# Kernel tuning notes

Hardware: AMD Instinct MI355X
Metric: run time of the kernel (lower is better)

Reference implementation:

```python
import jax, jax.numpy as jnp
import numpy as np

N_NODES = 100000
N_EDGES = 1600000
IN_CH = 64
HID = 64
OUT_CH = 16
T = 1.0


def _gat_layer(x, edge_index, W, b, t):
    # x: [N, d_in]; W: [d_out, d_in] (torch Linear weight layout); b: [d_out]
    N = x.shape[0]
    loop = jnp.arange(N, dtype=edge_index.dtype)
    src = jnp.concatenate([edge_index[0], loop])  # add self loops
    dst = jnp.concatenate([edge_index[1], loop])
    h = x @ W.T  # [N, d_out]
    x_i = h[dst]  # target node features per edge
    x_j = h[src]  # source node features per edge
    alpha = jnp.sum(x_i * x_j, axis=-1)  # [E']
    alpha = jnp.where(alpha > 0, jnp.asarray(t, h.dtype), jnp.asarray(-t, h.dtype))
    # segment softmax grouped by edge_index[0] (source), faithful to original
    m = jax.ops.segment_max(alpha, src, num_segments=N)
    e = jnp.exp(alpha - m[src])
    s = jax.ops.segment_sum(e, src, num_segments=N)
    w = e / s[src]
    msg = x_j * w[:, None]
    out = jax.ops.segment_sum(msg, dst, num_segments=N)  # scatter-add to target
    return out + b


def setup_inputs() -> dict:
    key = jax.random.key(0)
    k1, k2, k3, k4 = jax.random.split(key, 4)
    x = jax.random.normal(k1, (N_NODES, IN_CH), dtype=jnp.float32)
    edge_index = jax.random.randint(k2, (2, N_EDGES), 0, N_NODES, dtype=jnp.int64)
    # xavier-uniform-ish linear weights, torch layout [out, in]
    lim1 = float(np.sqrt(6.0 / (IN_CH + HID)))
    W1 = jax.random.uniform(k3, (HID, IN_CH), jnp.float32, -lim1, lim1)
    lim2 = float(np.sqrt(6.0 / (HID + OUT_CH)))
    W2 = jax.random.uniform(k4, (OUT_CH, HID), jnp.float32, -lim2, lim2)
    b1 = jnp.zeros((HID,), jnp.float32)
    b2 = jnp.zeros((OUT_CH,), jnp.float32)
    return {"x": x, "edge_index": edge_index, "W1": W1, "b1": b1, "W2": W2, "b2": b2}


def reference(x, edge_index, W1, b1, W2, b2):
    h = _gat_layer(x, edge_index, W1, b1, T)
    h = jax.nn.relu(h)
    h = _gat_layer(h, edge_index, W2, b2, T)
    return jax.nn.log_softmax(h, axis=1)
```

## Files before the change

kernel.cpp:

```cpp
#include <hip/hip_runtime.h>

#define EXPC 0.13533528323661270f
#define REP 8
#define CHUNK 16384

__global__ void zero_i32(int* __restrict__ p, int n) {
  int i = blockIdx.x * blockDim.x + threadIdx.x;
  if (i < n) p[i] = 0;
}

template <bool RELU_IN>
__global__ void __launch_bounds__(256, 1)
gemm64_k(const float* __restrict__ x, const float* __restrict__ W,
         float* __restrict__ h, int N) {
  __shared__ float xs[64][68];
  __shared__ float wt[64][68];
  const int t = threadIdx.x;
  const int r0 = blockIdx.x * 64;
  for (int i = t; i < 4096; i += 256) {
    int c = i >> 6, k = i & 63;
    wt[k][c] = W[i];
  }
  for (int s = t; s < 1024; s += 256) {
    int r = s >> 4, c4 = (s & 15) << 2;
    float4 v = make_float4(0.f, 0.f, 0.f, 0.f);
    if (r0 + r < N) {
      v = *(const float4*)(x + (size_t)(r0 + r) * 64 + c4);
      if (RELU_IN) {
        v.x = fmaxf(v.x, 0.f); v.y = fmaxf(v.y, 0.f);
        v.z = fmaxf(v.z, 0.f); v.w = fmaxf(v.w, 0.f);
      }
    }
    *(float4*)(&xs[r][c4]) = v;
  }
  __syncthreads();
  const int ty = t >> 4, tx = t & 15;
  float acc[4][4] = {};
  for (int kk = 0; kk < 64; kk += 4) {
    float4 a[4], w[4];
#pragma unroll
    for (int i = 0; i < 4; i++) a[i] = *(const float4*)(&xs[4 * ty + i][kk]);
#pragma unroll
    for (int m = 0; m < 4; m++) w[m] = *(const float4*)(&wt[kk + m][4 * tx]);
#pragma unroll
    for (int i = 0; i < 4; i++) {
      acc[i][0] = fmaf(a[i].x, w[0].x, fmaf(a[i].y, w[1].x,
                  fmaf(a[i].z, w[2].x, fmaf(a[i].w, w[3].x, acc[i][0]))));
      acc[i][1] = fmaf(a[i].x, w[0].y, fmaf(a[i].y, w[1].y,
                  fmaf(a[i].z, w[2].y, fmaf(a[i].w, w[3].y, acc[i][1]))));
      acc[i][2] = fmaf(a[i].x, w[0].z, fmaf(a[i].y, w[1].z,
                  fmaf(a[i].z, w[2].z, fmaf(a[i].w, w[3].z, acc[i][2]))));
      acc[i][3] = fmaf(a[i].x, w[0].w, fmaf(a[i].y, w[1].w,
                  fmaf(a[i].z, w[2].w, fmaf(a[i].w, w[3].w, acc[i][3]))));
    }
  }
#pragma unroll
  for (int i = 0; i < 4; i++) {
    int row = r0 + 4 * ty + i;
    if (row < N)
      *(float4*)(h + (size_t)row * 64 + 4 * tx) =
          make_float4(acc[i][0], acc[i][1], acc[i][2], acc[i][3]);
  }
}

template <bool RELU_IN>
__global__ void __launch_bounds__(256, 2)
gemm16_k(const float* __restrict__ x, const float* __restrict__ W,
         float* __restrict__ h, int N) {
  __shared__ float xs[64][68];
  __shared__ float wt[64][20];
  const int t = threadIdx.x;
  const int r0 = blockIdx.x * 64;
  for (int i = t; i < 1024; i += 256) {
    int c = i >> 6, k = i & 63;
    wt[k][c] = W[i];
  }
  for (int s = t; s < 1024; s += 256) {
    int r = s >> 4, c4 = (s & 15) << 2;
    float4 v = make_float4(0.f, 0.f, 0.f, 0.f);
    if (r0 + r < N) {
      v = *(const float4*)(x + (size_t)(r0 + r) * 64 + c4);
      if (RELU_IN) {
        v.x = fmaxf(v.x, 0.f); v.y = fmaxf(v.y, 0.f);
        v.z = fmaxf(v.z, 0.f); v.w = fmaxf(v.w, 0.f);
      }
    }
    *(float4*)(&xs[r][c4]) = v;
  }
  __syncthreads();
  const int r = t >> 2, j = (t & 3) << 2;
  float4 acc = make_float4(0.f, 0.f, 0.f, 0.f);
  for (int k = 0; k < 64; k++) {
    float a = xs[r][k];
    float4 w = *(const float4*)(&wt[k][j]);
    acc.x = fmaf(a, w.x, acc.x);
    acc.y = fmaf(a, w.y, acc.y);
    acc.z = fmaf(a, w.z, acc.z);
    acc.w = fmaf(a, w.w, acc.w);
  }
  int row = r0 + r;
  if (row < N) *(float4*)(h + (size_t)row * 16 + j) = acc;
}

__global__ void passA_k(const int* __restrict__ ei, int* __restrict__ chd,
                        int* __restrict__ chs, int E, int Et) {
  __shared__ int ld[512], ls[512];
  int t = threadIdx.x;
  for (int i = t; i < 512; i += 256) { ld[i] = 0; ls[i] = 0; }
  __syncthreads();
  int base = blockIdx.x * CHUNK;
  int end = base + CHUNK; if (end > Et) end = Et;
  for (int e = base + t; e < end; e += 256) {
    int s, d;
    if (e < E) { s = ei[e]; d = ei[E + e]; } else { s = e - E; d = s; }
    atomicAdd(&ld[d >> 8], 1);
    atomicAdd(&ls[s >> 8], 1);
  }
  __syncthreads();
  for (int i = t; i < 512; i += 256) {
    if (ld[i]) atomicAdd(chd + i, ld[i]);
    if (ls[i]) atomicAdd(chs + i, ls[i]);
  }
}

__global__ void scan2_k(const int* __restrict__ chd, const int* __restrict__ chs,
                        int* __restrict__ cbd, int* __restrict__ cbs,
                        int* __restrict__ cud, int* __restrict__ cus, int NB) {
  __shared__ int l[512];
  int t = threadIdx.x;
  for (int pass = 0; pass < 2; ++pass) {
    const int* src = pass ? chs : chd;
    int* db = pass ? cbs : cbd;
    int* dc = pass ? cus : cud;
    int v = (t < NB) ? src[t] : 0;
    l[t] = v;
    __syncthreads();
    for (int o = 1; o < 512; o <<= 1) {
      int a = (t >= o) ? l[t - o] : 0;
      __syncthreads();
      l[t] += a;
      __syncthreads();
    }
    if (t < NB) { int e = l[t] - v; db[t] = e; dc[t] = e; }
    __syncthreads();
  }
}

__global__ void passB_k(const int* __restrict__ ei, int* __restrict__ cud,
                        int* __restrict__ cus, int* __restrict__ part_dst,
                        unsigned char* __restrict__ part_src, int E, int Et) {
  __shared__ int cntd[512], cnts[512], based[512], bases[512];
  int t = threadIdx.x;
  for (int i = t; i < 512; i += 256) { cntd[i] = 0; cnts[i] = 0; }
  __syncthreads();
  int base = blockIdx.x * CHUNK;
  int end = base + CHUNK; if (end > Et) end = Et;
  for (int e = base + t; e < end; e += 256) {
    int s, d;
    if (e < E) { s = ei[e]; d = ei[E + e]; } else { s = e - E; d = s; }
    atomicAdd(&cntd[d >> 8], 1);
    atomicAdd(&cnts[s >> 8], 1);
  }
  __syncthreads();
  for (int i = t; i < 512; i += 256) {
    based[i] = cntd[i] ? atomicAdd(cud + i, cntd[i]) : 0;
    bases[i] = cnts[i] ? atomicAdd(cus + i, cnts[i]) : 0;
    cntd[i] = 0; cnts[i] = 0;
  }
  __syncthreads();
  for (int e = base + t; e < end; e += 256) {
    int s, d;
    if (e < E) { s = ei[e]; d = ei[E + e]; } else { s = e - E; d = s; }
    int bd = d >> 8, bs = s >> 8;
    int rd = atomicAdd(&cntd[bd], 1);
    int rs = atomicAdd(&cnts[bs], 1);
    part_dst[based[bd] + rd] = s | ((d & 255) << 17);
    part_src[bases[bs] + rs] = (unsigned char)(s & 255);
  }
}

__global__ void passC_k(const int* __restrict__ part_dst, const int* __restrict__ cbd,
                        const int* __restrict__ chd, int* __restrict__ csr_src,
                        int* __restrict__ in_deg, int* __restrict__ off, int N) {
  __shared__ int hist[256], loff[256], rank[256];
  int b = blockIdx.x, t = threadIdx.x;
  int segbase = cbd[b], segcnt = chd[b];
  hist[t] = 0; rank[t] = 0;
  __syncthreads();
  for (int i = t; i < segcnt; i += 256)
    atomicAdd(&hist[part_dst[segbase + i] >> 17], 1);
  __syncthreads();
  int x = hist[t];
  loff[t] = x;
  __syncthreads();
  for (int o = 1; o < 256; o <<= 1) {
    int a = (t >= o) ? loff[t - o] : 0;
    __syncthreads();
    loff[t] += a;
    __syncthreads();
  }
  int excl = loff[t] - x;
  int node = (b << 8) + t;
  if (node < N) { in_deg[node] = x; off[node] = segbase + excl; }
  __syncthreads();
  loff[t] = excl;
  __syncthreads();
  for (int i = t; i < segcnt; i += 256) {
    int rec = part_dst[segbase + i];
    int dl = rec >> 17;
    int r = atomicAdd(&rank[dl], 1);
    csr_src[segbase + loff[dl] + r] = rec & 0x1FFFF;
  }
}

__global__ void passCs_k(const unsigned char* __restrict__ part_src,
                         const int* __restrict__ cbs, const int* __restrict__ chs,
                         int* __restrict__ deg, int N) {
  __shared__ int hist[256];
  int b = blockIdx.x, t = threadIdx.x;
  int segbase = cbs[b], segcnt = chs[b];
  hist[t] = 0;
  __syncthreads();
  for (int i = t; i < segcnt; i += 256)
    atomicAdd(&hist[part_src[segbase + i]], 1);
  __syncthreads();
  int node = (b << 8) + t;
  if (node < N) deg[node] = hist[t];
}

template <int D>
__global__ void alpha_csr_k(const int* __restrict__ csr_src, const int* __restrict__ off,
                            const int* __restrict__ indeg, const float* __restrict__ h,
                            unsigned char* __restrict__ flagb, int* __restrict__ pos_rep,
                            int N) {
  const int G = D / 4;
  int t = blockIdx.x * 256 + threadIdx.x;
  int node = t / G;
  int c = t & (G - 1);
  if (node >= N) return;
  int* pos = pos_rep + (blockIdx.x & (REP - 1)) * N;
  const float4 hd = *(const float4*)(h + (size_t)node * D + c * 4);
  int j = off[node];
  int je = j + indeg[node];
  for (; j < je; ++j) {
    int s = csr_src[j];
    float4 hs = *(const float4*)(h + (size_t)s * D + c * 4);
    float p = fmaf(hs.x, hd.x, fmaf(hs.y, hd.y, fmaf(hs.z, hd.z, hs.w * hd.w)));
#pragma unroll
    for (int o = G / 2; o > 0; o >>= 1) p += __shfl_xor(p, o);
    if (c == 0) {
      bool pz = p > 0.f;
      flagb[j] = (unsigned char)pz;
      if (pz) atomicAdd(pos + s, 1);
    }
  }
}

__global__ void denom_k(const int* __restrict__ pos_rep, const int* __restrict__ deg,
                        float* __restrict__ dinv, int N) {
  int i = blockIdx.x * blockDim.x + threadIdx.x;
  if (i >= N) return;
  int p = 0;
#pragma unroll
  for (int r = 0; r < REP; r++) p += pos_rep[r * N + i];
  int dg = deg[i];
  dinv[i] = (p > 0) ? 1.f / ((float)p + (float)(dg - p) * EXPC)
                    : 1.f / (EXPC * (float)dg);
}

template <int D, bool FUSE_LSM>
__global__ void gather_csr_k(const int* __restrict__ csr_src, const int* __restrict__ off,
                             const int* __restrict__ indeg,
                             const unsigned char* __restrict__ flagb,
                             const float* __restrict__ dinv, const float* __restrict__ h,
                             const float* __restrict__ b, float* __restrict__ outp, int N) {
  const int G = D / 4;
  int t = blockIdx.x * 256 + threadIdx.x;
  int node = t / G;
  int c = t & (G - 1);
  if (node >= N) return;
  float4 acc = *(const float4*)(b + c * 4);
  int j = off[node];
  int je = j + indeg[node];
  for (; j < je; ++j) {
    int s = csr_src[j];
    float w = (flagb[j] ? 1.f : EXPC) * dinv[s];
    float4 hv = *(const float4*)(h + (size_t)s * D + c * 4);
    acc.x = fmaf(w, hv.x, acc.x);
    acc.y = fmaf(w, hv.y, acc.y);
    acc.z = fmaf(w, hv.z, acc.z);
    acc.w = fmaf(w, hv.w, acc.w);
  }
  if (FUSE_LSM) {
    float m = fmaxf(fmaxf(acc.x, acc.y), fmaxf(acc.z, acc.w));
    m = fmaxf(m, __shfl_xor(m, 1));
    m = fmaxf(m, __shfl_xor(m, 2));
    float s = expf(acc.x - m) + expf(acc.y - m) + expf(acc.z - m) + expf(acc.w - m);
    s += __shfl_xor(s, 1);
    s += __shfl_xor(s, 2);
    float lse = m + logf(s);
    acc.x -= lse; acc.y -= lse; acc.z -= lse; acc.w -= lse;
  }
  *(float4*)(outp + (size_t)node * D + c * 4) = acc;
}

extern "C" void kernel_launch(void* const* d_in, const int* in_sizes, int n_in,
                              void* d_out, int out_size, void* d_ws, size_t ws_size,
                              hipStream_t stream) {
  const float* x = (const float*)d_in[0];
  const int* ei = (const int*)d_in[1];
  const float* W1 = (const float*)d_in[2];
  const float* b1 = (const float*)d_in[3];
  const float* W2 = (const float*)d_in[4];
  const float* b2 = (const float*)d_in[5];
  float* out = (float*)d_out;

  const int N = in_sizes[0] / 64;
  const int E = in_sizes[1] / 2;
  const int Et = E + N;
  const int B = 256;
  const int nbN = (N + B - 1) / B;
  const int nbT = (N + 63) / 64;
  const int NB = (N + 255) >> 8;
  const int nbP = (Et + CHUNK - 1) / CHUNK;

  char* ws = (char*)d_ws;
  float* h1 = (float*)ws;    ws += (size_t)N * 64 * 4;
  float* agg1 = (float*)ws;  ws += (size_t)N * 64 * 4;
  int* deg = (int*)ws;       ws += (size_t)N * 4;
  int* in_deg = (int*)ws;    ws += (size_t)N * 4;
  int* off = (int*)ws;       ws += (size_t)N * 4;
  float* dinv = (float*)ws;  ws += (size_t)N * 4;
  int* chd = (int*)ws;       ws += 512 * 4;
  int* chs = (int*)ws;       ws += 512 * 4;
  int* cbd = (int*)ws;       ws += 512 * 4;
  int* cbs = (int*)ws;       ws += 512 * 4;
  int* cud = (int*)ws;       ws += 512 * 4;
  int* cus = (int*)ws;       ws += 512 * 4;
  int* csr_src = (int*)ws;   ws += (size_t)Et * 4;
  char* P = ws;              ws += (size_t)Et * 4 + (size_t)Et;
  int* part_dst = (int*)P;
  unsigned char* part_src = (unsigned char*)(P + (size_t)Et * 4);
  int* pos_rep = (int*)P;
  unsigned char* flagb = (unsigned char*)(P + (size_t)REP * N * 4);

  hipLaunchKernelGGL(zero_i32, dim3(4), dim3(B), 0, stream, chd, 1024);
  hipLaunchKernelGGL(passA_k, dim3(nbP), dim3(B), 0, stream, ei, chd, chs, E, Et);
  hipLaunchKernelGGL(scan2_k, dim3(1), dim3(512), 0, stream, chd, chs, cbd, cbs, cud, cus, NB);
  hipLaunchKernelGGL(passB_k, dim3(nbP), dim3(B), 0, stream, ei, cud, cus,
                     part_dst, part_src, E, Et);
  hipLaunchKernelGGL(passC_k, dim3(NB), dim3(B), 0, stream, part_dst, cbd, chd,
                     csr_src, in_deg, off, N);
  hipLaunchKernelGGL(passCs_k, dim3(NB), dim3(B), 0, stream, part_src, cbs, chs, deg, N);

  hipLaunchKernelGGL((gemm64_k<false>), dim3(nbT), dim3(B), 0, stream, x, W1, h1, N);
  hipLaunchKernelGGL(zero_i32, dim3((REP * N + B - 1) / B), dim3(B), 0, stream,
                     pos_rep, REP * N);
  hipLaunchKernelGGL((alpha_csr_k<64>), dim3(((size_t)N * 16 + B - 1) / B), dim3(B), 0,
                     stream, csr_src, off, in_deg, h1, flagb, pos_rep, N);
  hipLaunchKernelGGL(denom_k, dim3(nbN), dim3(B), 0, stream, pos_rep, deg, dinv, N);
  hipLaunchKernelGGL((gather_csr_k<64, false>), dim3(((size_t)N * 16 + B - 1) / B), dim3(B),
                     0, stream, csr_src, off, in_deg, flagb, dinv, h1, b1, agg1, N);

  float* h2 = h1;
  hipLaunchKernelGGL((gemm16_k<true>), dim3(nbT), dim3(B), 0, stream, agg1, W2, h2, N);
  hipLaunchKernelGGL(zero_i32, dim3((REP * N + B - 1) / B), dim3(B), 0, stream,
                     pos_rep, REP * N);
  hipLaunchKernelGGL((alpha_csr_k<16>), dim3(((size_t)N * 4 + B - 1) / B), dim3(B), 0,
                     stream, csr_src, off, in_deg, h2, flagb, pos_rep, N);
  hipLaunchKernelGGL(denom_k, dim3(nbN), dim3(B), 0, stream, pos_rep, deg, dinv, N);
  hipLaunchKernelGGL((gather_csr_k<16, true>), dim3(((size_t)N * 4 + B - 1) / B), dim3(B),
                     0, stream, csr_src, off, in_deg, flagb, dinv, h2, b2, out, N);
}
```

Before: 523.1 us.

## Prescale features by softmax denominator and unroll CSR edge loops by four

Result: faster. 486.5 us (-7.0%).

```diff
diff --git a/kernel.cpp b/kernel.cpp
--- a/kernel.cpp
+++ b/kernel.cpp
@@ -242,6 +242,32 @@
   const float4 hd = *(const float4*)(h + (size_t)node * D + c * 4);
   int j = off[node];
   int je = j + indeg[node];
+  for (; j + 4 <= je; j += 4) {
+    int s0 = csr_src[j], s1 = csr_src[j + 1], s2 = csr_src[j + 2], s3 = csr_src[j + 3];
+    float4 a0 = *(const float4*)(h + (size_t)s0 * D + c * 4);
+    float4 a1 = *(const float4*)(h + (size_t)s1 * D + c * 4);
+    float4 a2 = *(const float4*)(h + (size_t)s2 * D + c * 4);
+    float4 a3 = *(const float4*)(h + (size_t)s3 * D + c * 4);
+    float p0 = fmaf(a0.x, hd.x, fmaf(a0.y, hd.y, fmaf(a0.z, hd.z, a0.w * hd.w)));
+    float p1 = fmaf(a1.x, hd.x, fmaf(a1.y, hd.y, fmaf(a1.z, hd.z, a1.w * hd.w)));
+    float p2 = fmaf(a2.x, hd.x, fmaf(a2.y, hd.y, fmaf(a2.z, hd.z, a2.w * hd.w)));
+    float p3 = fmaf(a3.x, hd.x, fmaf(a3.y, hd.y, fmaf(a3.z, hd.z, a3.w * hd.w)));
+#pragma unroll
+    for (int o = G / 2; o > 0; o >>= 1) {
+      p0 += __shfl_xor(p0, o);
+      p1 += __shfl_xor(p1, o);
+      p2 += __shfl_xor(p2, o);
+      p3 += __shfl_xor(p3, o);
+    }
+    if (c == 0) {
+      bool z0 = p0 > 0.f, z1 = p1 > 0.f, z2 = p2 > 0.f, z3 = p3 > 0.f;
+      flagb[j] = z0; flagb[j + 1] = z1; flagb[j + 2] = z2; flagb[j + 3] = z3;
+      if (z0) atomicAdd(pos + s0, 1);
+      if (z1) atomicAdd(pos + s1, 1);
+      if (z2) atomicAdd(pos + s2, 1);
+      if (z3) atomicAdd(pos + s3, 1);
+    }
+  }
   for (; j < je; ++j) {
     int s = csr_src[j];
     float4 hs = *(const float4*)(h + (size_t)s * D + c * 4);
@@ -256,23 +282,35 @@
   }
 }
 
-__global__ void denom_k(const int* __restrict__ pos_rep, const int* __restrict__ deg,
-                        float* __restrict__ dinv, int N) {
-  int i = blockIdx.x * blockDim.x + threadIdx.x;
-  if (i >= N) return;
-  int p = 0;
-#pragma unroll
-  for (int r = 0; r < REP; r++) p += pos_rep[r * N + i];
-  int dg = deg[i];
-  dinv[i] = (p > 0) ? 1.f / ((float)p + (float)(dg - p) * EXPC)
-                    : 1.f / (EXPC * (float)dg);
+template <int D>
+__global__ void denom_scale_k(const int* __restrict__ pos_rep, const int* __restrict__ deg,
+                              float* __restrict__ h, int N) {
+  const int G = D / 4;
+  int t = blockIdx.x * 256 + threadIdx.x;
+  int node = t / G;
+  int c = t & (G - 1);
+  if (node >= N) return;
+  float dinv = 0.f;
+  if (c == 0) {
+    int p = 0;
+#pragma unroll
+    for (int r = 0; r < REP; r++) p += pos_rep[r * N + node];
+    int dg = deg[node];
+    dinv = (p > 0) ? 1.f / ((float)p + (float)(dg - p) * EXPC)
+                   : 1.f / (EXPC * (float)dg);
+  }
+  dinv = __shfl(dinv, 0, G);
+  float4* hp = (float4*)(h + (size_t)node * D + c * 4);
+  float4 v = *hp;
+  v.x *= dinv; v.y *= dinv; v.z *= dinv; v.w *= dinv;
+  *hp = v;
 }
 
 template <int D, bool FUSE_LSM>
 __global__ void gather_csr_k(const int* __restrict__ csr_src, const int* __restrict__ off,
                              const int* __restrict__ indeg,
                              const unsigned char* __restrict__ flagb,
-                             const float* __restrict__ dinv, const float* __restrict__ h,
+                             const float* __restrict__ h,
                              const float* __restrict__ b, float* __restrict__ outp, int N) {
   const int G = D / 4;
   int t = blockIdx.x * 256 + threadIdx.x;
@@ -282,9 +320,24 @@
   float4 acc = *(const float4*)(b + c * 4);
   int j = off[node];
   int je = j + indeg[node];
+  for (; j + 4 <= je; j += 4) {
+    int s0 = csr_src[j], s1 = csr_src[j + 1], s2 = csr_src[j + 2], s3 = csr_src[j + 3];
+    float w0 = flagb[j] ? 1.f : EXPC;
+    float w1 = flagb[j + 1] ? 1.f : EXPC;
+    float w2 = flagb[j + 2] ? 1.f : EXPC;
+    float w3 = flagb[j + 3] ? 1.f : EXPC;
+    float4 v0 = *(const float4*)(h + (size_t)s0 * D + c * 4);
+    float4 v1 = *(const float4*)(h + (size_t)s1 * D + c * 4);
+    float4 v2 = *(const float4*)(h + (size_t)s2 * D + c * 4);
+    float4 v3 = *(const float4*)(h + (size_t)s3 * D + c * 4);
+    acc.x = fmaf(w0, v0.x, fmaf(w1, v1.x, fmaf(w2, v2.x, fmaf(w3, v3.x, acc.x))));
+    acc.y = fmaf(w0, v0.y, fmaf(w1, v1.y, fmaf(w2, v2.y, fmaf(w3, v3.y, acc.y))));
+    acc.z = fmaf(w0, v0.z, fmaf(w1, v1.z, fmaf(w2, v2.z, fmaf(w3, v3.z, acc.z))));
+    acc.w = fmaf(w0, v0.w, fmaf(w1, v1.w, fmaf(w2, v2.w, fmaf(w3, v3.w, acc.w))));
+  }
   for (; j < je; ++j) {
     int s = csr_src[j];
-    float w = (flagb[j] ? 1.f : EXPC) * dinv[s];
+    float w = flagb[j] ? 1.f : EXPC;
     float4 hv = *(const float4*)(h + (size_t)s * D + c * 4);
     acc.x = fmaf(w, hv.x, acc.x);
     acc.y = fmaf(w, hv.y, acc.y);
@@ -319,7 +372,6 @@
   const int E = in_sizes[1] / 2;
   const int Et = E + N;
   const int B = 256;
-  const int nbN = (N + B - 1) / B;
   const int nbT = (N + 63) / 64;
   const int NB = (N + 255) >> 8;
   const int nbP = (Et + CHUNK - 1) / CHUNK;
@@ -330,7 +382,6 @@
   int* deg = (int*)ws;       ws += (size_t)N * 4;
   int* in_deg = (int*)ws;    ws += (size_t)N * 4;
   int* off = (int*)ws;       ws += (size_t)N * 4;
-  float* dinv = (float*)ws;  ws += (size_t)N * 4;
   int* chd = (int*)ws;       ws += 512 * 4;
   int* chs = (int*)ws;       ws += 512 * 4;
   int* cbd = (int*)ws;       ws += 512 * 4;
@@ -358,9 +409,10 @@
                      pos_rep, REP * N);
   hipLaunchKernelGGL((alpha_csr_k<64>), dim3(((size_t)N * 16 + B - 1) / B), dim3(B), 0,
                      stream, csr_src, off, in_deg, h1, flagb, pos_rep, N);
-  hipLaunchKernelGGL(denom_k, dim3(nbN), dim3(B), 0, stream, pos_rep, deg, dinv, N);
+  hipLaunchKernelGGL((denom_scale_k<64>), dim3(((size_t)N * 16 + B - 1) / B), dim3(B), 0,
+                     stream, pos_rep, deg, h1, N);
   hipLaunchKernelGGL((gather_csr_k<64, false>), dim3(((size_t)N * 16 + B - 1) / B), dim3(B),
-                     0, stream, csr_src, off, in_deg, flagb, dinv, h1, b1, agg1, N);
+                     0, stream, csr_src, off, in_deg, flagb, h1, b1, agg1, N);
 
   float* h2 = h1;
   hipLaunchKernelGGL((gemm16_k<true>), dim3(nbT), dim3(B), 0, stream, agg1, W2, h2, N);
@@ -368,7 +420,8 @@
                      pos_rep, REP * N);
   hipLaunchKernelGGL((alpha_csr_k<16>), dim3(((size_t)N * 4 + B - 1) / B), dim3(B), 0,
                      stream, csr_src, off, in_deg, h2, flagb, pos_rep, N);
-  hipLaunchKernelGGL(denom_k, dim3(nbN), dim3(B), 0, stream, pos_rep, deg, dinv, N);
+  hipLaunchKernelGGL((denom_scale_k<16>), dim3(((size_t)N * 4 + B - 1) / B), dim3(B), 0,
+                     stream, pos_rep, deg, h2, N);
   hipLaunchKernelGGL((gather_csr_k<16, true>), dim3(((size_t)N * 4 + B - 1) / B), dim3(B),
-                     0, stream, csr_src, off, in_deg, flagb, dinv, h2, b2, out, N);
-}
+                     0, stream, csr_src, off, in_deg, flagb, h2, b2, out, N);
+}
```
